# Kernel optimization log

Measured on AMD Instinct MI355X. Metric: run time of the kernel, lower is better.

Reference implementation:

```python
import jax, jax.numpy as jnp
import numpy as np

B, DIM, OC, H, W, HEADS = 4, 128, 128, 128, 128, 8
L = H * W
_BN_INV = 1.0 / (1.0 + 1e-5) ** 0.5  # eval-mode BN: running_mean=0, running_var=1


def conv2d(x, w, b=None, groups=1, pad=0):
    y = jax.lax.conv_general_dilated(
        x, w, (1, 1), [(pad, pad), (pad, pad)],
        dimension_numbers=('NCHW', 'OIHW', 'NCHW'),
        feature_group_count=groups)
    if b is not None:
        y = y + b[None, :, None, None]
    return y


def bn(x, g, b):
    return x * (g * _BN_INV)[None, :, None, None] + b[None, :, None, None]


def ln(x, g, b, eps=1e-5):
    m = jnp.mean(x, -1, keepdims=True)
    v = jnp.mean((x - m) ** 2, -1, keepdims=True)
    return (x - m) * jax.lax.rsqrt(v + eps) * g + b


def rope_tables(h, w, c, base=10000.0):
    k_max = c // 4
    theta = 1.0 / base ** (np.arange(k_max, dtype=np.float32) / k_max)
    gi, gj = np.meshgrid(np.arange(h, dtype=np.float32),
                         np.arange(w, dtype=np.float32), indexing='ij')
    ang = np.concatenate([gi[..., None] * theta, gj[..., None] * theta], -1)  # (h,w,c//2)
    return jnp.asarray(np.cos(ang)), jnp.asarray(np.sin(ang))


def apply_rope(x, cs, sn):  # x: (b,h,w,c); consecutive pairs = (re, im)
    xr, xi = x[..., 0::2], x[..., 1::2]
    return jnp.stack([cs * xr - sn * xi, sn * xr + cs * xi], -1).reshape(x.shape)


def linear_attn(x, qk_w, qk_b, lepe_w, lepe_b, h, w):
    b, n, c = x.shape
    hd = c // HEADS
    qk = x @ qk_w.T + qk_b
    q = jax.nn.elu(qk[..., :c]) + 1.0
    k = jax.nn.elu(qk[..., c:]) + 1.0
    cs, sn = rope_tables(h, w, c)

    def heads(t):  # (b,n,c) -> (b,HEADS,n,hd)
        return t.reshape(b, n, HEADS, hd).transpose(0, 2, 1, 3)

    q_r = heads(apply_rope(q.reshape(b, h, w, c), cs, sn).reshape(b, n, c))
    k_r = heads(apply_rope(k.reshape(b, h, w, c), cs, sn).reshape(b, n, c))
    qh, kh, vh = heads(q), heads(k), heads(x)
    k_mean = jnp.mean(kh, axis=2, keepdims=True)                      # (b,Hd,1,hd)
    z = 1.0 / (jnp.einsum('bhnd,bhmd->bhnm', qh, k_mean) + 1e-6)      # (b,Hd,n,1)
    s = n ** -0.5
    kv = jnp.einsum('bhnd,bhne->bhde', k_r * s, vh * s)               # (b,Hd,hd,hd)
    out = jnp.einsum('bhnd,bhde->bhne', q_r, kv) * z
    out = out.transpose(0, 2, 1, 3).reshape(b, n, c)
    v_img = x.reshape(b, h, w, c).transpose(0, 3, 1, 2)
    lepe = conv2d(v_img, lepe_w, lepe_b, groups=c, pad=1)
    return out + lepe.transpose(0, 2, 3, 1).reshape(b, n, c)


def fmt_block(xb, fw1, fb1, f_g, f_be, fw2, fb2, n_g, n_be):
    t = jnp.fft.fft2(xb)                                              # (B,C,H,W) complex
    wgt = jax.nn.relu(bn(conv2d(t.real, fw1, fb1), f_g, f_be))
    wgt = jax.nn.sigmoid(conv2d(wgt, fw2, fb2))
    f = jnp.abs(jnp.fft.ifft2(wgt * t))
    f = jax.nn.relu(bn(f, n_g, n_be))
    return f.reshape(f.shape[0], f.shape[1], -1).transpose(0, 2, 1)   # (B,L,C)


def _forward(x, c1_w, c1_b, c1_g, c1_be, cpe1_w, cpe1_b,
             fw1, fb1, f_g, f_be, fw2, fb2, nbn_g, nbn_be,
             ln1_g, ln1_b, d3w1, d3b1, d3w2, d5w1, d5b1, d5w2,
             ap_w, ap_b, ip2_w, ip2_b, dwc2_w, dwc2_b,
             qk_w, qk_b, lepe_w, lepe_b, op_w, op_b,
             cpe2_w, cpe2_b, ln2_g, ln2_b,
             ffn_w1, ffn_b1, ffn_w2, ffn_b2, po_w,
             red_w, red_b, red_g, red_be):
    Bb, C, Hh, Ww = x.shape
    Ll = Hh * Ww
    to_img = lambda t: t.reshape(Bb, Hh, Ww, C).transpose(0, 3, 1, 2)   # (B,L,C)->(B,C,H,W)
    to_seq = lambda t: t.transpose(0, 2, 3, 1).reshape(Bb, Ll, -1)       # (B,C,H,W)->(B,L,C)

    x_0 = jax.nn.relu(bn(conv2d(x, c1_w, c1_b), c1_g, c1_be))           # (B,OC,H,W)
    xt = to_seq(x + conv2d(x, cpe1_w, cpe1_b, groups=C, pad=1))
    shortcut = xt
    fmt1 = fmt_block(to_img(xt), fw1, fb1, f_g, f_be, fw2, fb2, nbn_g, nbn_be)

    x_s = ln(xt, ln1_g, ln1_b)
    xs_img = to_img(x_s)
    x_s3 = conv2d(conv2d(xs_img, d3w1, d3b1), d3w2, None, groups=C // 2, pad=1)
    x_s5 = conv2d(conv2d(xs_img, d5w1, d5b1), d5w2, None, groups=C // 2, pad=2)
    act_res = jax.nn.silu(to_seq(conv2d(xs_img, ap_w, ap_b)))

    def branch(t):  # (B,C/2,H,W) -> (B,L,C/2)
        t = conv2d(t, ip2_w, ip2_b)
        t = jax.nn.silu(conv2d(t, dwc2_w, dwc2_b, groups=C // 2, pad=1))
        return to_seq(t)

    a3 = linear_attn(branch(x_s3), qk_w, qk_b, lepe_w, lepe_b, Hh, Ww)
    a5 = linear_attn(branch(x_s5), qk_w, qk_b, lepe_w, lepe_b, Hh, Ww)
    xs = jnp.concatenate([a3, a5], -1)
    xs = to_seq(conv2d(to_img(xs * act_res), op_w, op_b))

    xt = shortcut + xs + fmt1
    xt = xt + to_seq(conv2d(to_img(xt), cpe2_w, cpe2_b, groups=C, pad=1))
    fmt2 = fmt_block(to_img(xt), fw1, fb1, f_g, f_be, fw2, fb2, nbn_g, nbn_be)
    h2 = ln(xt, ln2_g, ln2_b)
    ffn = jax.nn.gelu(h2 @ ffn_w1.T + ffn_b1, approximate=False) @ ffn_w2.T + ffn_b2
    xt = xt + ffn + fmt2

    xo = conv2d(to_img(xt), po_w)                                        # (B,OC,H,W)
    cat = jnp.concatenate([x_0, xo], 1)
    return jax.nn.relu(bn(conv2d(cat, red_w, red_b), red_g, red_be)) + x_0


def setup_inputs():
    key = jax.random.key(0)
    it = iter(jax.random.split(key, 64))

    def w(shape, s=0.05):
        return jax.random.normal(next(it), shape, jnp.float32) * s

    d, oc = DIM, OC
    ones = lambda n: jnp.ones((n,), jnp.float32)
    zeros = lambda n: jnp.zeros((n,), jnp.float32)
    return {
        'x': jax.random.normal(next(it), (B, d, H, W), jnp.float32),
        'c1_w': w((oc, d, 1, 1)), 'c1_b': w((oc,), 0.01), 'c1_g': ones(oc), 'c1_be': zeros(oc),
        'cpe1_w': w((d, 1, 3, 3)), 'cpe1_b': w((d,), 0.01),
        'fw1': w((d // 16, d, 1, 1)), 'fb1': w((d // 16,), 0.01),
        'f_g': ones(d // 16), 'f_be': zeros(d // 16),
        'fw2': w((d, d // 16, 1, 1)), 'fb2': w((d,), 0.01),
        'nbn_g': ones(d), 'nbn_be': zeros(d),
        'ln1_g': ones(d), 'ln1_b': zeros(d),
        'd3w1': w((d, d, 1, 1)), 'd3b1': w((d,), 0.01), 'd3w2': w((d // 2, 2, 3, 3)),
        'd5w1': w((d, d, 1, 1)), 'd5b1': w((d,), 0.01), 'd5w2': w((d // 2, 2, 5, 5)),
        'ap_w': w((d, d, 1, 1)), 'ap_b': w((d,), 0.01),
        'ip2_w': w((d // 2, d // 2, 1, 1)), 'ip2_b': w((d // 2,), 0.01),
        'dwc2_w': w((d // 2, 1, 3, 3)), 'dwc2_b': w((d // 2,), 0.01),
        'qk_w': w((d, d // 2)), 'qk_b': w((d,), 0.01),
        'lepe_w': w((d // 2, 1, 3, 3)), 'lepe_b': w((d // 2,), 0.01),
        'op_w': w((d, d, 1, 1)), 'op_b': w((d,), 0.01),
        'cpe2_w': w((d, 1, 3, 3)), 'cpe2_b': w((d,), 0.01),
        'ln2_g': ones(d), 'ln2_b': zeros(d),
        'ffn_w1': w((4, d)), 'ffn_b1': w((4,), 0.01),
        'ffn_w2': w((d, 4)), 'ffn_b2': w((d,), 0.01),
        'po_w': w((oc, d, 1, 1)),
        'red_w': w((oc, 2 * oc, 1, 1)), 'red_b': w((oc,), 0.01),
        'red_g': ones(oc), 'red_be': zeros(oc),
    }


def reference(x, c1_w, c1_b, c1_g, c1_be, cpe1_w, cpe1_b,
              fw1, fb1, f_g, f_be, fw2, fb2, nbn_g, nbn_be,
              ln1_g, ln1_b, d3w1, d3b1, d3w2, d5w1, d5b1, d5w2,
              ap_w, ap_b, ip2_w, ip2_b, dwc2_w, dwc2_b,
              qk_w, qk_b, lepe_w, lepe_b, op_w, op_b,
              cpe2_w, cpe2_b, ln2_g, ln2_b,
              ffn_w1, ffn_b1, ffn_w2, ffn_b2, po_w,
              red_w, red_b, red_g, red_be):
    return _forward(x, c1_w, c1_b, c1_g, c1_be, cpe1_w, cpe1_b,
                    fw1, fb1, f_g, f_be, fw2, fb2, nbn_g, nbn_be,
                    ln1_g, ln1_b, d3w1, d3b1, d3w2, d5w1, d5b1, d5w2,
                    ap_w, ap_b, ip2_w, ip2_b, dwc2_w, dwc2_b,
                    qk_w, qk_b, lepe_w, lepe_b, op_w, op_b,
                    cpe2_w, cpe2_b, ln2_g, ln2_b,
                    ffn_w1, ffn_b1, ffn_w2, ffn_b2, po_w,
                    red_w, red_b, red_g, red_be)
```

## Files before the change

kernel.cpp:

```cpp
#include <hip/hip_runtime.h>
#include <math.h>

typedef unsigned short bf16_t;
typedef __attribute__((ext_vector_type(8))) short short8;
typedef __attribute__((ext_vector_type(4))) float f32x4;

#define B_ 4
#define C_ 128
#define H_ 128
#define W_ 128
#define L_ (H_*W_)
#define NS  ((size_t)B_*L_*C_)
#define NH  ((size_t)B_*L_*64)
#define NSP ((size_t)L_*C_)
#define PI_F 3.14159265358979323846f
#define BN_INV 0.9999950000374997f
#define THETA_SC 0.8304820237218406f
#define TOTW 157148
#define W16SHIFT 107548

#define W2_ 66
#define L2_ (128*W2_)

__device__ __forceinline__ float ldf(bf16_t v){ return __uint_as_float(((unsigned)v)<<16); }
__device__ __forceinline__ bf16_t f2b(float f){
  unsigned u = __float_as_uint(f);
  u += 0x7fffu + ((u>>16)&1u);
  return (bf16_t)(u>>16);
}

#define WGSZ ((size_t)B_*8*L2_)
#define WGSLOT ((size_t)B_*8*L_)
#define ACCSZ 2304
#define CWSZ 157184
#define CW16SZF 78592
#define WSF (6*NS + 3*NH + WGSLOT + ACCSZ + CWSZ + CW16SZF + 16)
__device__ float g_ws[WSF];

__global__ void k_probe(const bf16_t* __restrict__ xb, int* __restrict__ flag){
  __shared__ int vote;
  if (threadIdx.x == 0) vote = 0;
  __syncthreads();
  int bad = 0;
  for (int i = threadIdx.x; i < 2048; i += 256) {
    float v = ldf(xb[2*i]);
    if (!(fabsf(v) < 1e6f)) bad = 1;
  }
  if (bad) atomicOr(&vote, 1);
  __syncthreads();
  if (threadIdx.x == 0) *flag = vote;
}

struct P47 { const void* p[47]; };
__device__ __constant__ int c_wsz[47] = {
  16384,128,128,128,1152,128,1024,8,8,8,1024,128,128,128,128,128,
  16384,128,1152,16384,128,3200,16384,128,4096,64,576,64,8192,128,
  576,64,16384,128,1152,128,128,128,512,4,512,128,16384,32768,128,128,128};

__global__ __launch_bounds__(256) void k_cvt(P47 ps, const int* __restrict__ flagp,
                                             float* __restrict__ dst){
  int g = blockIdx.x*256 + threadIdx.x;
  if (g >= TOTW) return;
  int fl = *flagp;
  int idx = 0, off = g;
  while (off >= c_wsz[idx]) { off -= c_wsz[idx]; idx++; }
  const void* s = ps.p[idx];
  dst[g] = fl ? ((const float*)s)[off] : ldf(((const bf16_t*)s)[off]);
}

__global__ __launch_bounds__(256) void k_cvt16(const float* __restrict__ src, bf16_t* __restrict__ dst){
  int g = blockIdx.x*256 + threadIdx.x;
  if (g >= TOTW) return;
  dst[g + (g >= W16SHIFT ? 4 : 0)] = f2b(src[g]);
}

__global__ void k_zero(float* p, int n){
  int i = blockIdx.x*256 + threadIdx.x;
  if (i < n) p[i] = 0.f;
}

__device__ __forceinline__ void tw_fwd(int lane, float* tc, float* ts) {
  sincosf(-PI_F * (float)lane * (1.f/64.f), &ts[0], &tc[0]);
  int i = 1;
  #pragma unroll
  for (int m = 32; m >= 1; m >>= 1, i++) {
    int k = lane & (m-1);
    sincosf(-PI_F * (float)k / (float)m, &ts[i], &tc[i]);
  }
}
__device__ __forceinline__ void tw_inv(int lane, float* tc, float* ts) {
  int i = 0;
  #pragma unroll
  for (int m = 1; m <= 32; m <<= 1, i++) {
    int k = lane & (m-1);
    sincosf(PI_F * (float)k / (float)m, &ts[i], &tc[i]);
  }
  sincosf(PI_F * (float)lane * (1.f/64.f), &ts[6], &tc[6]);
}

__device__ __forceinline__ void fft128_fwd(float& lor, float& loi, float& hir, float& hii,
                                           int lane, const float* tc, const float* ts) {
  {
    float s = ts[0], c = tc[0];
    float ar = lor, ai = loi;
    float dr = ar - hir, di = ai - hii;
    lor = ar + hir; loi = ai + hii;
    hir = dr*c - di*s; hii = dr*s + di*c;
  }
  int i = 1;
  #pragma unroll
  for (int m = 32; m >= 1; m >>= 1, i++) {
    float s = ts[i], c = tc[i];
    bool up = (lane & m) != 0;
    {
      float orr = __shfl_xor(lor, m), oii = __shfl_xor(loi, m);
      float sr = lor + orr, si = loi + oii;
      float dr = orr - lor, di = oii - loi;
      float tr = dr*c - di*s, ti = dr*s + di*c;
      lor = up ? tr : sr; loi = up ? ti : si;
    }
    {
      float orr = __shfl_xor(hir, m), oii = __shfl_xor(hii, m);
      float sr = hir + orr, si = hii + oii;
      float dr = orr - hir, di = oii - hii;
      float tr = dr*c - di*s, ti = dr*s + di*c;
      hir = up ? tr : sr; hii = up ? ti : si;
    }
  }
}

__device__ __forceinline__ void fft128_inv(float& lor, float& loi, float& hir, float& hii,
                                           int lane, const float* tc, const float* ts) {
  int i = 0;
  #pragma unroll
  for (int m = 1; m <= 32; m <<= 1, i++) {
    float s = ts[i], c = tc[i];
    bool up = (lane & m) != 0;
    {
      float orr = __shfl_xor(lor, m), oii = __shfl_xor(loi, m);
      float qr = orr*c - oii*s, qi = orr*s + oii*c;
      float lo_r = lor + qr, lo_i = loi + qi;
      float mr = lor*c - loi*s, mi = lor*s + loi*c;
      float up_r = orr - mr, up_i = oii - mi;
      lor = up ? up_r : lo_r; loi = up ? up_i : lo_i;
    }
    {
      float orr = __shfl_xor(hir, m), oii = __shfl_xor(hii, m);
      float qr = orr*c - oii*s, qi = orr*s + oii*c;
      float lo_r = hir + qr, lo_i = hii + qi;
      float mr = hir*c - hii*s, mi = hir*s + hii*c;
      float up_r = orr - mr, up_i = oii - mi;
      hir = up ? up_r : lo_r; hii = up ? up_i : lo_i;
    }
  }
  {
    float s = ts[6], c = tc[6];
    float qr = hir*c - hii*s, qi = hir*s + hii*c;
    float pr = lor, pi = loi;
    lor = pr + qr; loi = pi + qi;
    hir = pr - qr; hii = pi - qi;
  }
}

__global__ __launch_bounds__(256) void k_fft_row_fwd_half(
    const float* __restrict__ in, float* __restrict__ re, float* __restrict__ im) {
  __shared__ float T[64*130];
  int tid = threadIdx.x;
  int bid = blockIdx.x;
  int ch = (bid & 1) * 64;
  int h  = (bid >> 1) & 127;
  int b  = bid >> 8;
  const float* ip = in + ((size_t)b*L_ + (size_t)h*128)*128 + ch;
  #pragma unroll
  for (int it = 0; it < 8; it++) {
    int idx = it*256 + tid;
    int c4 = (idx & 15)*4, w = idx >> 4;
    float4 v = *(const float4*)(ip + (size_t)w*128 + c4);
    T[(c4+0)*130 + w] = v.x;
    T[(c4+1)*130 + w] = v.y;
    T[(c4+2)*130 + w] = v.z;
    T[(c4+3)*130 + w] = v.w;
  }
  __syncthreads();
  int lane = tid & 63, wv = tid >> 6;
  int rb = (int)(__brev((unsigned)lane) >> 26);
  int pe = (64 - lane) & 63;
  int po = 63 - lane;
  float tc[7], ts[7];
  tw_fwd(lane, tc, ts);
  #pragma unroll
  for (int t = 0; t < 8; t++) {
    int ca = wv*16 + 2*t, cb = ca + 1;
    float lor = T[ca*130 + lane],      loi = T[cb*130 + lane];
    float hir = T[ca*130 + 64 + lane], hii = T[cb*130 + 64 + lane];
    fft128_fwd(lor, loi, hir, hii, lane, tc, ts);
    float er  = __shfl(lor, rb), ei  = __shfl(loi, rb);
    float our = __shfl(hir, rb), oui = __shfl(hii, rb);
    float per = __shfl(er, pe),  pei = __shfl(ei, pe);
    float por = __shfl(our, po), poi = __shfl(oui, po);
    float ae_r = 0.5f*(er + per),  ae_i = 0.5f*(ei - pei);
    float be_r = 0.5f*(ei + pei),  be_i = 0.5f*(per - er);
    float ao_r = 0.5f*(our + por), ao_i = 0.5f*(oui - poi);
    float bo_r = 0.5f*(oui + poi), bo_i = 0.5f*(por - our);
    if (lane == 32) { ao_r = 0.f; ao_i = 0.f; bo_r = 0.f; bo_i = 0.f; }
    if (lane <= 32) {
      size_t ba = (size_t)(b*128 + ch + ca)*L2_ + (size_t)h*W2_ + 2*lane;
      size_t bb = (size_t)(b*128 + ch + cb)*L2_ + (size_t)h*W2_ + 2*lane;
      *(float2*)(re + ba) = make_float2(ae_r, ao_r);
      *(float2*)(im + ba) = make_float2(ae_i, ao_i);
      *(float2*)(re + bb) = make_float2(be_r, bo_r);
      *(float2*)(im + bb) = make_float2(be_i, bo_i);
    }
  }
}

__global__ __launch_bounds__(256) void k_fft_col_fwd_h(float* __restrict__ re, float* __restrict__ im) {
  __shared__ float Lre[128][34];
  __shared__ float Lim[128][34];
  int tid = threadIdx.x;
  size_t img = blockIdx.x >> 1;
  int w0 = (blockIdx.x & 1) * 33;
  float* rp = re + img * (size_t)L2_ + w0;
  float* ip = im + img * (size_t)L2_ + w0;
  for (int i = tid; i < 4224; i += 256) {
    int h = i / 33, wl = i - h*33;
    Lre[h][wl] = rp[(size_t)h*W2_ + wl];
    Lim[h][wl] = ip[(size_t)h*W2_ + wl];
  }
  __syncthreads();
  int lane = tid & 63, wv = tid >> 6;
  float tc[7], ts[7];
  tw_fwd(lane, tc, ts);
  for (int col = wv; col < 33; col += 4) {
    float lor = Lre[lane][col], loi = Lim[lane][col];
    float hir = Lre[lane+64][col], hii = Lim[lane+64][col];
    fft128_fwd(lor, loi, hir, hii, lane, tc, ts);
    Lre[lane][col]=lor; Lim[lane][col]=loi;
    Lre[lane+64][col]=hir; Lim[lane+64][col]=hii;
  }
  __syncthreads();
  for (int i = tid; i < 4224; i += 256) {
    int h = i / 33, wl = i - h*33;
    rp[(size_t)h*W2_ + wl] = Lre[h][wl];
    ip[(size_t)h*W2_ + wl] = Lim[h][wl];
  }
}

__global__ __launch_bounds__(256) void k_fft_col_inv_scaled_h(
    float* __restrict__ re, float* __restrict__ im,
    const float* __restrict__ wg1, const float* __restrict__ fw2,
    const float* __restrict__ fb2) {
  __shared__ float Lre[128][34];
  __shared__ float Lim[128][34];
  __shared__ float w2r[8];
  int tid = threadIdx.x;
  size_t img = blockIdx.x >> 1;
  int c = (int)(img & 127);
  int b = (int)(img >> 7);
  int w0 = (blockIdx.x & 1) * 33;
  if (tid < 8) w2r[tid] = fw2[c*8 + tid];
  float b2 = fb2[c];
  float* rp = re + img * (size_t)L2_ + w0;
  float* ip = im + img * (size_t)L2_ + w0;
  const float* wgp = wg1 + (size_t)b*8*L2_ + w0;
  __syncthreads();
  for (int i = tid; i < 4224; i += 256) {
    int h = i / 33, wl = i - h*33;
    size_t p = (size_t)h*W2_ + wl;
    float a = b2;
    #pragma unroll
    for (int o = 0; o < 8; o++) a += w2r[o] * wgp[(size_t)o*L2_ + p];
    float wgt = 1.f/(1.f+expf(-a));
    Lre[h][wl] = rp[p] * wgt;
    Lim[h][wl] = ip[p] * wgt;
  }
  __syncthreads();
  int lane = tid & 63, wv = tid >> 6;
  float tc[7], ts[7];
  tw_inv(lane, tc, ts);
  for (int col = wv; col < 33; col += 4) {
    float lor = Lre[lane][col], loi = Lim[lane][col];
    float hir = Lre[lane+64][col], hii = Lim[lane+64][col];
    fft128_inv(lor, loi, hir, hii, lane, tc, ts);
    Lre[lane][col]=lor*(1.f/128.f); Lim[lane][col]=loi*(1.f/128.f);
    Lre[lane+64][col]=hir*(1.f/128.f); Lim[lane+64][col]=hii*(1.f/128.f);
  }
  __syncthreads();
  for (int i = tid; i < 4224; i += 256) {
    int h = i / 33, wl = i - h*33;
    rp[(size_t)h*W2_ + wl] = Lre[h][wl];
    ip[(size_t)h*W2_ + wl] = Lim[h][wl];
  }
}

__global__ __launch_bounds__(256) void k_fft_row_inv_abs_seq_h(
    const float* __restrict__ re, const float* __restrict__ im,
    const float* __restrict__ ng, const float* __restrict__ nbe,
    const float* __restrict__ add1, const float* __restrict__ add2,
    float* __restrict__ out) {
  __shared__ float S[64*132];
  int tid = threadIdx.x;
  int bid = blockIdx.x;
  int ch = (bid & 1) * 64;
  int h  = (bid >> 1) & 127;
  int b  = bid >> 8;
  {
    const float* rbase = re + (size_t)(b*128 + ch)*L2_ + (size_t)h*W2_;
    const float* ibase = im + (size_t)(b*128 + ch)*L2_ + (size_t)h*W2_;
    for (int i = tid; i < 64*66; i += 256) {
      int c = i / 66, v = i - c*66;
      S[c*132 + v]      = rbase[(size_t)c*L2_ + v];
      S[c*132 + 66 + v] = ibase[(size_t)c*L2_ + v];
    }
  }
  __syncthreads();
  int lane = tid & 63, wv = tid >> 6;
  int rb = (int)(__brev((unsigned)lane) >> 26);
  int vlo = 2*rb, vhi = vlo + 1;
  float tc[7], ts[7];
  tw_inv(lane, tc, ts);
  float rr[8][4];
  #pragma unroll
  for (int t = 0; t < 8; t++) {
    int ca = wv*16 + 2*t, cb = ca + 1;
    const float* Sa = S + ca*132;
    const float* Sb = S + cb*132;
    float lor, loi, hir, hii;
    if (vlo <= 64) {
      float ar = Sa[vlo], ai = Sa[66+vlo], br = Sb[vlo], bi = Sb[66+vlo];
      lor = ar - bi; loi = ai + br;
    } else {
      int u = 128 - vlo;
      float ar = Sa[u], ai = Sa[66+u], br = Sb[u], bi = Sb[66+u];
      lor = ar + bi; loi = br - ai;
    }
    if (vhi <= 64) {
      float ar = Sa[vhi], ai = Sa[66+vhi], br = Sb[vhi], bi = Sb[66+vhi];
      hir = ar - bi; hii = ai + br;
    } else {
      int u = 128 - vhi;
      float ar = Sa[u], ai = Sa[66+u], br = Sb[u], bi = Sb[66+u];
      hir = ar + bi; hii = br - ai;
    }
    fft128_inv(lor, loi, hir, hii, lane, tc, ts);
    rr[t][0] = fabsf(lor);
    rr[t][1] = fabsf(loi);
    rr[t][2] = fabsf(hir);
    rr[t][3] = fabsf(hii);
  }
  __syncthreads();
  float* T = S;
  #pragma unroll
  for (int t = 0; t < 8; t++) {
    int ca = wv*16 + 2*t, cb = ca + 1;
    float sga = ng[ch+ca]*BN_INV, sba = nbe[ch+ca];
    float sgb = ng[ch+cb]*BN_INV, sbb = nbe[ch+cb];
    T[ca*130 + lane]      = fmaxf(rr[t][0]*(1.f/128.f)*sga + sba, 0.f);
    T[cb*130 + lane]      = fmaxf(rr[t][1]*(1.f/128.f)*sgb + sbb, 0.f);
    T[ca*130 + 64 + lane] = fmaxf(rr[t][2]*(1.f/128.f)*sga + sba, 0.f);
    T[cb*130 + 64 + lane] = fmaxf(rr[t][3]*(1.f/128.f)*sgb + sbb, 0.f);
  }
  __syncthreads();
  size_t sb0 = ((size_t)b*L_ + (size_t)h*128)*128 + ch;
  #pragma unroll
  for (int it = 0; it < 8; it++) {
    int idx = it*256 + tid;
    int c4 = (idx & 15)*4, w = idx >> 4;
    size_t off = sb0 + (size_t)w*128 + c4;
    float4 v;
    v.x = T[(c4+0)*130 + w];
    v.y = T[(c4+1)*130 + w];
    v.z = T[(c4+2)*130 + w];
    v.w = T[(c4+3)*130 + w];
    float4 x1 = *(const float4*)(add1 + off);
    float4 x2 = *(const float4*)(add2 + off);
    v.x += x1.x + x2.x; v.y += x1.y + x2.y;
    v.z += x1.z + x2.z; v.w += x1.w + x2.w;
    *(float4*)(out + off) = v;
  }
}

__global__ __launch_bounds__(256) void k_freq1_h(const float* __restrict__ tre,
    const float* __restrict__ fw1, const float* __restrict__ fb1,
    const float* __restrict__ fg, const float* __restrict__ fbe,
    float* __restrict__ wg1) {
  __shared__ float w1s[1024];
  int tid = threadIdx.x;
  for (int i = tid; i < 1024; i += 256) w1s[i] = fw1[i];
  __syncthreads();
  size_t g = (size_t)blockIdx.x*256 + tid;
  int p = (int)(g % L2_);
  int b = (int)(g / L2_);
  const float* tp = tre + (size_t)b*128*L2_ + p;
  float acc[8];
  #pragma unroll
  for (int o = 0; o < 8; o++) acc[o] = 0.f;
  for (int c = 0; c < 128; c++) {
    float v = tp[(size_t)c*L2_];
    #pragma unroll
    for (int o = 0; o < 8; o++) acc[o] += w1s[o*128+c]*v;
  }
  size_t ob = (size_t)b*8*L2_ + p;
  #pragma unroll
  for (int o = 0; o < 8; o++) {
    float v = (acc[o] + fb1[o]) * (fg[o]*BN_INV) + fbe[o];
    wg1[ob + (size_t)o*L2_] = fmaxf(v, 0.f);
  }
}

template<bool DUAL>
__global__ void k_p2s(const void* __restrict__ src, float* __restrict__ dst,
                      const float* __restrict__ add1, const float* __restrict__ add2,
                      const int* __restrict__ flagp) {
  __shared__ float tile[32][33];
  int fl = DUAL ? *flagp : 1;
  int b = blockIdx.z;
  int p0 = blockIdx.x*32, c0 = blockIdx.y*32;
  int tx = threadIdx.x, ty = threadIdx.y;
  size_t base_in = (size_t)b*NSP;
  #pragma unroll
  for (int k = 0; k < 4; k++) {
    size_t off = base_in + (size_t)(c0+ty+8*k)*L_ + p0 + tx;
    float v;
    if (DUAL && !fl) v = ldf(((const bf16_t*)src)[off]);
    else             v = ((const float*)src)[off];
    tile[ty+8*k][tx] = v;
  }
  __syncthreads();
  size_t base = (size_t)b*NSP;
  #pragma unroll
  for (int k = 0; k < 4; k++) {
    size_t idx = base + (size_t)(p0+ty+8*k)*C_ + c0 + tx;
    float v = tile[tx][ty+8*k];
    if (add1) v += add1[idx];
    if (add2) v += add2[idx];
    dst[idx] = v;
  }
}

template<int CC, int MODE>
__global__ __launch_bounds__(256) void k_dw3(const float* __restrict__ in,
    const float* __restrict__ w, const float* __restrict__ bias,
    float* __restrict__ out) {
  __shared__ float wl[9*CC];
  int tid = threadIdx.x;
  for (int i = tid; i < 9*CC; i += 256) {
    int tap = i / CC, ch = i % CC;
    wl[i] = w[ch*9 + tap];
  }
  __syncthreads();
  size_t g = (size_t)blockIdx.x*256 + tid;
  int c = (int)(g & (CC-1));
  float wr[9];
  #pragma unroll
  for (int t = 0; t < 9; t++) wr[t] = wl[t*CC + c];
  size_t s = g / CC;
  int w0 = (int)(s & 31) * 4;
  int hp = (int)((s >> 5) & 127);
  int b  = (int)(s >> 12);
  const float* ip = in + (size_t)b*L_*CC + c;
  float bi = bias[c];
  float a0 = bi, a1 = bi, a2 = bi, a3 = bi;
  #pragma unroll
  for (int dh = -1; dh <= 1; dh++) {
    int h2 = hp + dh;
    if ((unsigned)h2 >= 128u) continue;
    const float* rp = ip + (size_t)h2*W_*CC;
    float px[6];
    #pragma unroll
    for (int x = 0; x < 6; x++) {
      int w2 = w0 - 1 + x;
      px[x] = ((unsigned)w2 < 128u) ? rp[(size_t)w2*CC] : 0.f;
    }
    #pragma unroll
    for (int dw = 0; dw < 3; dw++) {
      float f = wr[(dh+1)*3 + dw];
      a0 += f*px[dw];   a1 += f*px[dw+1];
      a2 += f*px[dw+2]; a3 += f*px[dw+3];
    }
  }
  size_t tb = (size_t)b*L_ + (size_t)hp*W_ + w0;
  if (MODE == 0) {
    out[(tb+0)*CC + c] = in[(tb+0)*CC + c] + a0;
    out[(tb+1)*CC + c] = in[(tb+1)*CC + c] + a1;
    out[(tb+2)*CC + c] = in[(tb+2)*CC + c] + a2;
    out[(tb+3)*CC + c] = in[(tb+3)*CC + c] + a3;
  } else {
    out[(tb+0)*CC + c] = a0 / (1.f + expf(-a0));
    out[(tb+1)*CC + c] = a1 / (1.f + expf(-a1));
    out[(tb+2)*CC + c] = a2 / (1.f + expf(-a2));
    out[(tb+3)*CC + c] = a3 / (1.f + expf(-a3));
  }
}

template<int K>
__global__ __launch_bounds__(256) void k_gconv(const float* __restrict__ in,
    const float* __restrict__ w, float* __restrict__ out) {
  __shared__ float wl[K*K*128];
  int tid = threadIdx.x;
  for (int i = tid; i < 128*K*K; i += 256) {
    int tap = i >> 7, ch = i & 127;
    wl[i] = w[ch*(K*K) + tap];
  }
  __syncthreads();
  size_t g = (size_t)blockIdx.x*256 + tid;
  int oc = (int)(g & 63);
  float wx[K*K], wy[K*K];
  #pragma unroll
  for (int t = 0; t < K*K; t++) {
    wx[t] = wl[t*128 + 2*oc];
    wy[t] = wl[t*128 + 2*oc + 1];
  }
  size_t s = g >> 6;
  int w0 = (int)(s & 31) * 4;
  int hp = (int)((s >> 5) & 127);
  int b  = (int)(s >> 12);
  const float* ip = in + (size_t)b*L_*128 + 2*oc;
  constexpr int P = K/2;
  float a0 = 0.f, a1 = 0.f, a2 = 0.f, a3 = 0.f;
  #pragma unroll
  for (int kh = 0; kh < K; kh++) {
    int h2 = hp + kh - P;
    if ((unsigned)h2 >= 128u) continue;
    const float* rp = ip + (size_t)h2*W_*128;
    float2 px[K+3];
    #pragma unroll
    for (int x = 0; x < K+3; x++) {
      int w2 = w0 - P + x;
      px[x] = ((unsigned)w2 < 128u) ? *(const float2*)(rp + (size_t)w2*128)
                                    : make_float2(0.f, 0.f);
    }
    #pragma unroll
    for (int kw = 0; kw < K; kw++) {
      float fx = wx[kh*K + kw], fy = wy[kh*K + kw];
      a0 += fx*px[kw+0].x + fy*px[kw+0].y;
      a1 += fx*px[kw+1].x + fy*px[kw+1].y;
      a2 += fx*px[kw+2].x + fy*px[kw+2].y;
      a3 += fx*px[kw+3].x + fy*px[kw+3].y;
    }
  }
  size_t tb = (size_t)b*L_ + (size_t)hp*W_ + w0;
  out[(tb+0)*64 + oc] = a0;
  out[(tb+1)*64 + oc] = a1;
  out[(tb+2)*64 + oc] = a2;
  out[(tb+3)*64 + oc] = a3;
}

template<int CIN, int COUT, int EPI, bool MUL>
__global__ __launch_bounds__(256) void k_mfma_tok(
    const float* __restrict__ in, const float* __restrict__ mulp,
    const bf16_t* __restrict__ W16, const float* __restrict__ bias,
    float* __restrict__ out) {
  constexpr int NO = COUT/16;
  int tid = threadIdx.x;
  int lane = tid & 63, wv = tid >> 6;
  int m = lane & 15, q = lane >> 4;
  size_t t0 = (size_t)blockIdx.x*64 + (size_t)wv*16;
  f32x4 acc[NO];
  #pragma unroll
  for (int i = 0; i < NO; i++) acc[i] = (f32x4){0.f,0.f,0.f,0.f};
  for (int k0 = 0; k0 < CIN; k0 += 32) {
    const float* ap = in + (t0 + m)*CIN + k0 + q*8;
    float4 a0 = *(const float4*)ap;
    float4 a1 = *(const float4*)(ap + 4);
    if (MUL) {
      const float* mp = mulp + (t0 + m)*CIN + k0 + q*8;
      float4 m0 = *(const float4*)mp;
      float4 m1 = *(const float4*)(mp + 4);
      a0.x*=m0.x; a0.y*=m0.y; a0.z*=m0.z; a0.w*=m0.w;
      a1.x*=m1.x; a1.y*=m1.y; a1.z*=m1.z; a1.w*=m1.w;
    }
    union { short s[8]; short8 v; } af;
    af.s[0]=(short)f2b(a0.x); af.s[1]=(short)f2b(a0.y);
    af.s[2]=(short)f2b(a0.z); af.s[3]=(short)f2b(a0.w);
    af.s[4]=(short)f2b(a1.x); af.s[5]=(short)f2b(a1.y);
    af.s[6]=(short)f2b(a1.z); af.s[7]=(short)f2b(a1.w);
    #pragma unroll
    for (int o = 0; o < NO; o++) {
      short8 bf = *(const short8*)(W16 + (size_t)(o*16 + m)*CIN + k0 + q*8);
      acc[o] = __builtin_amdgcn_mfma_f32_16x16x32_bf16(af.v, bf, acc[o], 0, 0, 0);
    }
  }
  #pragma unroll
  for (int o = 0; o < NO; o++) {
    float bv = (EPI >= 1) ? bias[o*16 + m] : 0.f;
    #pragma unroll
    for (int r = 0; r < 4; r++) {
      int row = q*4 + r;
      float v = acc[o][r] + bv;
      if (EPI == 2) v = v / (1.f + expf(-v));
      if (EPI == 3) v = v > 0.f ? v + 1.f : expf(v);
      out[(t0 + row)*COUT + o*16 + m] = v;
    }
  }
}

__global__ __launch_bounds__(256) void k_mfma_c1(
    const float* __restrict__ in, const bf16_t* __restrict__ W16,
    const float* __restrict__ bias, const float* __restrict__ gam,
    const float* __restrict__ bet, float* __restrict__ out) {
  constexpr int NO = 8;
  int tid = threadIdx.x;
  int lane = tid & 63, wv = tid >> 6;
  int m = lane & 15, q = lane >> 4;
  size_t t0 = (size_t)blockIdx.x*64 + (size_t)wv*16;
  f32x4 acc[NO];
  #pragma unroll
  for (int i = 0; i < NO; i++) acc[i] = (f32x4){0.f,0.f,0.f,0.f};
  for (int k0 = 0; k0 < 128; k0 += 32) {
    const float* ap = in + (t0 + m)*128 + k0 + q*8;
    float4 a0 = *(const float4*)ap;
    float4 a1 = *(const float4*)(ap + 4);
    union { short s[8]; short8 v; } af;
    af.s[0]=(short)f2b(a0.x); af.s[1]=(short)f2b(a0.y);
    af.s[2]=(short)f2b(a0.z); af.s[3]=(short)f2b(a0.w);
    af.s[4]=(short)f2b(a1.x); af.s[5]=(short)f2b(a1.y);
    af.s[6]=(short)f2b(a1.z); af.s[7]=(short)f2b(a1.w);
    #pragma unroll
    for (int o = 0; o < NO; o++) {
      short8 bf = *(const short8*)(W16 + (size_t)(o*16 + m)*128 + k0 + q*8);
      acc[o] = __builtin_amdgcn_mfma_f32_16x16x32_bf16(af.v, bf, acc[o], 0, 0, 0);
    }
  }
  #pragma unroll
  for (int o = 0; o < NO; o++) {
    int oc = o*16 + m;
    float bi = bias[oc], gm = gam[oc]*BN_INV, be = bet[oc];
    #pragma unroll
    for (int r = 0; r < 4; r++) {
      int row = q*4 + r;
      float v = acc[o][r] + bi;
      out[(t0 + row)*128 + oc] = fmaxf(v*gm + be, 0.f);
    }
  }
}

__global__ __launch_bounds__(256) void k_mfma_red(
    const float* __restrict__ x0s, const float* __restrict__ xo,
    const bf16_t* __restrict__ W16, const float* __restrict__ bias,
    const float* __restrict__ gam, const float* __restrict__ bet,
    void* __restrict__ out, const int* __restrict__ flagp) {
  __shared__ float T[128*65];
  constexpr int NO = 8;
  int fl = *flagp;
  int tid = threadIdx.x;
  int lane = tid & 63, wv = tid >> 6;
  int m = lane & 15, q = lane >> 4;
  size_t t0 = (size_t)blockIdx.x*64;
  size_t tw = t0 + (size_t)wv*16;
  f32x4 acc[NO];
  #pragma unroll
  for (int i = 0; i < NO; i++) acc[i] = (f32x4){0.f,0.f,0.f,0.f};
  for (int k0 = 0; k0 < 256; k0 += 32) {
    const float* src = (k0 < 128) ? (x0s + (tw + m)*128 + k0)
                                  : (xo  + (tw + m)*128 + (k0 - 128));
    float4 a0 = *(const float4*)(src + q*8);
    float4 a1 = *(const float4*)(src + q*8 + 4);
    union { short s[8]; short8 v; } af;
    af.s[0]=(short)f2b(a0.x); af.s[1]=(short)f2b(a0.y);
    af.s[2]=(short)f2b(a0.z); af.s[3]=(short)f2b(a0.w);
    af.s[4]=(short)f2b(a1.x); af.s[5]=(short)f2b(a1.y);
    af.s[6]=(short)f2b(a1.z); af.s[7]=(short)f2b(a1.w);
    #pragma unroll
    for (int o = 0; o < NO; o++) {
      short8 bf = *(const short8*)(W16 + (size_t)(o*16 + m)*256 + k0 + q*8);
      acc[o] = __builtin_amdgcn_mfma_f32_16x16x32_bf16(af.v, bf, acc[o], 0, 0, 0);
    }
  }
  #pragma unroll
  for (int ot = 0; ot < NO; ot++) {
    int o = ot*16 + m;
    float bi = bias[o], gm = gam[o]*BN_INV, be = bet[o];
    #pragma unroll
    for (int r = 0; r < 4; r++) {
      int row = q*4 + r;
      float v = acc[ot][r] + bi;
      v = fmaxf(v*gm + be, 0.f);
      v += x0s[(tw + row)*128 + o];
      T[o*65 + wv*16 + row] = v;
    }
  }
  __syncthreads();
  int b = (int)(t0 >> 14);
  int p0 = (int)(t0 & (L_-1));
  if (!fl) {
    bf16_t* op = (bf16_t*)out;
    for (int i = tid; i < 8192; i += 256) {
      int o = i >> 6, tk = i & 63;
      op[((size_t)b*128 + o)*L_ + p0 + tk] = f2b(T[o*65 + tk]);
    }
  } else {
    float* op = (float*)out;
    for (int i = tid; i < 8192; i += 256) {
      int o = i >> 6, tk = i & 63;
      op[((size_t)b*128 + o)*L_ + p0 + tk] = T[o*65 + tk];
    }
  }
}

__global__ __launch_bounds__(256) void k_ln(const float* __restrict__ in,
    const float* __restrict__ g, const float* __restrict__ be, float* __restrict__ out) {
  int tid = threadIdx.x, lane = tid & 63;
  size_t t = (size_t)blockIdx.x*4 + (tid >> 6);
  const float* row = in + t*128;
  float2 v = *(const float2*)(row + lane*2);
  float s = v.x + v.y, ss = v.x*v.x + v.y*v.y;
  #pragma unroll
  for (int m = 1; m < 64; m <<= 1) { s += __shfl_xor(s, m); ss += __shfl_xor(ss, m); }
  float mean = s*(1.f/128.f);
  float inv = rsqrtf(ss*(1.f/128.f) - mean*mean + 1e-5f);
  float2 o;
  o.x = (v.x-mean)*inv*g[lane*2]   + be[lane*2];
  o.y = (v.y-mean)*inv*g[lane*2+1] + be[lane*2+1];
  *(float2*)(out + t*128 + lane*2) = o;
}

__global__ __launch_bounds__(256) void k_ln_ffn(const float* __restrict__ in,
    const float* __restrict__ g, const float* __restrict__ be,
    const float* __restrict__ w1, const float* __restrict__ b1,
    const float* __restrict__ w2, const float* __restrict__ b2,
    float* __restrict__ out) {
  int tid = threadIdx.x, lane = tid & 63;
  size_t t = (size_t)blockIdx.x*4 + (tid >> 6);
  const float* row = in + t*128;
  float2 v = *(const float2*)(row + lane*2);
  float s = v.x + v.y, ss = v.x*v.x + v.y*v.y;
  #pragma unroll
  for (int m = 1; m < 64; m <<= 1) { s += __shfl_xor(s, m); ss += __shfl_xor(ss, m); }
  float mean = s*(1.f/128.f);
  float inv = rsqrtf(ss*(1.f/128.f) - mean*mean + 1e-5f);
  float hx = (v.x-mean)*inv*g[lane*2]   + be[lane*2];
  float hy = (v.y-mean)*inv*g[lane*2+1] + be[lane*2+1];
  float hp0 = hx*w1[0*128+lane*2] + hy*w1[0*128+lane*2+1];
  float hp1 = hx*w1[1*128+lane*2] + hy*w1[1*128+lane*2+1];
  float hp2 = hx*w1[2*128+lane*2] + hy*w1[2*128+lane*2+1];
  float hp3 = hx*w1[3*128+lane*2] + hy*w1[3*128+lane*2+1];
  #pragma unroll
  for (int m = 1; m < 64; m <<= 1) {
    hp0 += __shfl_xor(hp0, m); hp1 += __shfl_xor(hp1, m);
    hp2 += __shfl_xor(hp2, m); hp3 += __shfl_xor(hp3, m);
  }
  float hv0, hv1, hv2, hv3;
  { float a = hp0 + b1[0]; hv0 = 0.5f*a*(1.f+erff(a*0.7071067811865476f)); }
  { float a = hp1 + b1[1]; hv1 = 0.5f*a*(1.f+erff(a*0.7071067811865476f)); }
  { float a = hp2 + b1[2]; hv2 = 0.5f*a*(1.f+erff(a*0.7071067811865476f)); }
  { float a = hp3 + b1[3]; hv3 = 0.5f*a*(1.f+erff(a*0.7071067811865476f)); }
  int cx = lane*2, cy = lane*2+1;
  float2 o;
  o.x = hv0*w2[cx*4+0] + hv1*w2[cx*4+1] + hv2*w2[cx*4+2] + hv3*w2[cx*4+3] + b2[cx];
  o.y = hv0*w2[cy*4+0] + hv1*w2[cy*4+1] + hv2*w2[cy*4+2] + hv3*w2[cy*4+3] + b2[cy];
  *(float2*)(out + t*128 + lane*2) = o;
}

__global__ __launch_bounds__(256) void k_kv(
    const float* __restrict__ qk, const float* __restrict__ v,
    float* __restrict__ akv_g, float* __restrict__ aks_g) {
  __shared__ float kvred[512];
  __shared__ float ksred[64];
  int tid = threadIdx.x;
  for (int i = tid; i < 512; i += 256) kvred[i] = 0.f;
  if (tid < 64) ksred[tid] = 0.f;
  __syncthreads();
  int lane = tid & 63, wv = tid >> 6;
  size_t t0 = (size_t)blockIdx.x * 64;
  int b = (int)(t0 >> 14);
  int pr = lane >> 1;
  float theta = exp2f(-(float)(pr & 15) * THETA_SC);
  bool use_i = pr < 16;
  int hbase = lane & 56;
  float akv[8];
  #pragma unroll
  for (int d = 0; d < 8; d++) akv[d] = 0.f;
  float aks = 0.f;
  for (int it = 0; it < 16; it++) {
    size_t t = t0 + (size_t)wv*16 + it;
    float k = qk[t*128 + 64 + lane];
    float xv = v[t*64 + lane];
    int l = (int)(t & (L_-1));
    float pos = use_i ? (float)(l >> 7) : (float)(l & 127);
    float sn, cs; sincosf(pos*theta, &sn, &cs);
    float kp = __shfl_xor(k, 1);
    float kr = (lane & 1) ? (sn*kp + cs*k) : (cs*k - sn*kp);
    #pragma unroll
    for (int d = 0; d < 8; d++) {
      float krd = __shfl(kr, hbase + d);
      akv[d] += krd * xv;
    }
    aks += k;
  }
  int h8 = lane >> 3, e = lane & 7;
  #pragma unroll
  for (int d = 0; d < 8; d++)
    atomicAdd(&kvred[h8*64 + d*8 + e], akv[d]);
  atomicAdd(&ksred[lane], aks);
  __syncthreads();
  for (int i = tid; i < 512; i += 256) atomicAdd(&akv_g[b*512 + i], kvred[i]);
  if (tid < 64) atomicAdd(&aks_g[b*64 + tid], ksred[tid]);
}

__global__ __launch_bounds__(256) void k_attn2(
    const float* __restrict__ qk, const float* __restrict__ x,
    const float* __restrict__ akv_g, const float* __restrict__ aks_g,
    const float* __restrict__ lw, const float* __restrict__ lb,
    float* __restrict__ out, int coff) {
  __shared__ float kv[512];
  __shared__ float km[64];
  __shared__ float lwl[576];
  int tid = threadIdx.x;
  size_t t0 = (size_t)blockIdx.x * 32;
  int b = (int)(t0 >> 14);
  const float invn = 1.f/16384.f;
  for (int i = tid; i < 512; i += 256) kv[i] = akv_g[b*512 + i]*invn;
  if (tid < 64) km[tid] = aks_g[b*64 + tid]*invn;
  for (int i = tid; i < 576; i += 256) lwl[i] = lw[i];
  __syncthreads();
  int lane = tid & 63, wv = tid >> 6;
  int pr = lane >> 1;
  float theta = exp2f(-(float)(pr & 15) * THETA_SC);
  bool use_i = pr < 16;
  int hbase = lane & 56, e = lane & 7;
  float lbv = lb[lane];
  const float* xb = x + ((size_t)b << 14) * 64;
  for (int it = 0; it < 8; it++) {
    size_t t = t0 + (size_t)wv*8 + it;
    int l = (int)(t & (L_-1));
    int ipos = l >> 7, jpos = l & 127;
    float q = qk[t*128 + lane];
    float p = q * km[lane];
    p += __shfl_xor(p, 1); p += __shfl_xor(p, 2); p += __shfl_xor(p, 4);
    float z = 1.f/(p + 1e-6f);
    float pos = use_i ? (float)ipos : (float)jpos;
    float sn, cs; sincosf(pos*theta, &sn, &cs);
    float qp = __shfl_xor(q, 1);
    float qr = (lane & 1) ? (sn*qp + cs*q) : (cs*q - sn*qp);
    float acc = 0.f;
    #pragma unroll
    for (int d = 0; d < 8; d++) {
      float qrd = __shfl(qr, hbase + d);
      acc += qrd * kv[hbase*8 + d*8 + e];
    }
    acc *= z;
    float lp = lbv;
    #pragma unroll
    for (int dh = -1; dh <= 1; dh++) {
      int h2 = ipos + dh; if ((unsigned)h2 >= 128u) continue;
      #pragma unroll
      for (int dw = -1; dw <= 1; dw++) {
        int w2 = jpos + dw; if ((unsigned)w2 >= 128u) continue;
        lp += lwl[lane*9 + (dh+1)*3 + (dw+1)] * xb[((size_t)(h2 << 7) + w2)*64 + lane];
      }
    }
    out[t*128 + coff + lane] = acc + lp;
  }
}

extern "C" void kernel_launch(void* const* d_in, const int* in_sizes, int n_in,
                              void* d_out, int out_size, void* d_ws, size_t ws_size,
                              hipStream_t stream) {
  (void)in_sizes; (void)n_in; (void)out_size;

  float* base;
  if (ws_size >= WSF * sizeof(float)) {
    base = (float*)d_ws;
  } else {
    void* p = nullptr;
    hipGetSymbolAddress(&p, HIP_SYMBOL(g_ws));
    base = (float*)p;
  }
  float* P0 = base;
  float* PA = base + 1*NS;
  float* PB = base + 2*NS;
  float* PC = base + 3*NS;
  float* PD = base + 4*NS;
  float* PF = base + 5*NS;
  float* H0 = base + 6*NS;
  float* H1 = H0 + NH;
  float* H2 = H1 + NH;
  float* WG = H2 + NH;
  float* ACC = WG + WGSLOT;
  float* CW  = ACC + ACCSZ;
  bf16_t* CW16 = (bf16_t*)(CW + CWSZ);
  int*   FLG = (int*)(CW + CWSZ + CW16SZF);

  static const int wsz[47] = {
    16384,128,128,128,1152,128,1024,8,8,8,1024,128,128,128,128,128,
    16384,128,1152,16384,128,3200,16384,128,4096,64,576,64,8192,128,
    576,64,16384,128,1152,128,128,128,512,4,512,128,16384,32768,128,128,128};
  int woff[47]; { int a = 0; for (int i = 0; i < 47; i++){ woff[i] = a; a += wsz[i]; } }
  const float* Wf[47]; for (int i = 0; i < 47; i++) Wf[i] = CW + woff[i];
  auto W16 = [&](int i){ return (const bf16_t*)(CW16 + woff[i] + (woff[i] >= W16SHIFT ? 4 : 0)); };
  const float *c1_b=Wf[1], *c1_g=Wf[2], *c1_be=Wf[3], *cpe1_w=Wf[4],
    *cpe1_b=Wf[5], *fw1=Wf[6], *fb1=Wf[7], *f_g=Wf[8], *f_be=Wf[9], *fw2=Wf[10],
    *fb2=Wf[11], *nbn_g=Wf[12], *nbn_be=Wf[13], *ln1_g=Wf[14], *ln1_b=Wf[15],
    *d3b1=Wf[17], *d3w2=Wf[18], *d5b1=Wf[20],
    *d5w2=Wf[21], *ap_b=Wf[23], *ip2_b=Wf[25],
    *dwc2_w=Wf[26], *dwc2_b=Wf[27], *qk_b=Wf[29], *lepe_w=Wf[30],
    *lepe_b=Wf[31], *op_b=Wf[33], *cpe2_w=Wf[34], *cpe2_b=Wf[35],
    *ln2_g=Wf[36], *ln2_b=Wf[37], *ffn_w1=Wf[38], *ffn_b1=Wf[39], *ffn_w2=Wf[40],
    *ffn_b2=Wf[41], *red_b=Wf[44], *red_g=Wf[45], *red_be=Wf[46];
  const bf16_t *c1_w16=W16(0), *d3w1_16=W16(16), *d5w1_16=W16(19), *ap_w16=W16(22),
    *ip2_w16=W16(24), *qk_w16=W16(28), *op_w16=W16(32), *po_w16=W16(42), *red_w16=W16(43);

  const void* x = d_in[0];

  k_probe<<<1, 256, 0, stream>>>((const bf16_t*)x, FLG);
  P47 ps; for (int i = 0; i < 47; i++) ps.p[i] = d_in[i+1];
  k_cvt<<<(TOTW+255)/256, 256, 0, stream>>>(ps, FLG, CW);
  k_cvt16<<<(TOTW+255)/256, 256, 0, stream>>>(CW, CW16);

  dim3 tgrid(512, 4, 4), tblk(32, 8);

  auto fmt_fused = [&](const float* seq_in, float* re, float* im,
                       const float* add1, const float* add2, float* outp) {
    k_fft_row_fwd_half<<<1024, 256, 0, stream>>>(seq_in, re, im);
    k_fft_col_fwd_h<<<1024, 256, 0, stream>>>(re, im);
    k_freq1_h<<<132, 256, 0, stream>>>(re, fw1, fb1, f_g, f_be, WG);
    k_fft_col_inv_scaled_h<<<1024, 256, 0, stream>>>(re, im, WG, fw2, fb2);
    k_fft_row_inv_abs_seq_h<<<1024, 256, 0, stream>>>(re, im, nbn_g, nbn_be, add1, add2, outp);
  };

  auto attn = [&](const float* brin, float* qkbuf, int coff) {
    k_zero<<<9, 256, 0, stream>>>(ACC, 2304);
    k_mfma_tok<64,128,3,false><<<1024, 256, 0, stream>>>(brin, nullptr, qk_w16, qk_b, qkbuf);
    k_kv<<<1024, 256, 0, stream>>>(qkbuf, brin, ACC, ACC + B_*512);
    k_attn2<<<2048, 256, 0, stream>>>(qkbuf, brin, ACC, ACC + B_*512, lepe_w, lepe_b, PF, coff);
  };

  k_p2s<true><<<tgrid, tblk, 0, stream>>>(x, PA, nullptr, nullptr, FLG);
  k_mfma_c1<<<1024, 256, 0, stream>>>(PA, c1_w16, c1_b, c1_g, c1_be, P0);
  k_dw3<128,0><<<8192, 256, 0, stream>>>(PA, cpe1_w, cpe1_b, PB);
  k_ln<<<16384, 256, 0, stream>>>(PB, ln1_g, ln1_b, PA);
  k_mfma_tok<128,128,1,false><<<1024, 256, 0, stream>>>(PA, nullptr, d3w1_16, d3b1, PD);
  k_gconv<3><<<4096, 256, 0, stream>>>(PD, d3w2, H0);
  k_mfma_tok<128,128,1,false><<<1024, 256, 0, stream>>>(PA, nullptr, d5w1_16, d5b1, PD);
  k_gconv<5><<<4096, 256, 0, stream>>>(PD, d5w2, H1);
  k_mfma_tok<128,128,2,false><<<1024, 256, 0, stream>>>(PA, nullptr, ap_w16, ap_b, PA);
  k_mfma_tok<64,64,1,false><<<1024, 256, 0, stream>>>(H0, nullptr, ip2_w16, ip2_b, H2);
  k_dw3<64,1><<<4096, 256, 0, stream>>>(H2, dwc2_w, dwc2_b, H0);
  attn(H0, PD, 0);
  k_mfma_tok<64,64,1,false><<<1024, 256, 0, stream>>>(H1, nullptr, ip2_w16, ip2_b, H2);
  k_dw3<64,1><<<4096, 256, 0, stream>>>(H2, dwc2_w, dwc2_b, H1);
  attn(H1, PD, 64);
  k_mfma_tok<128,128,1,true><<<1024, 256, 0, stream>>>(PF, PA, op_w16, op_b, PF);
  fmt_fused(PB, PC, PD, PB, PF, PB);
  k_dw3<128,0><<<8192, 256, 0, stream>>>(PB, cpe2_w, cpe2_b, PC);
  k_ln_ffn<<<16384, 256, 0, stream>>>(PC, ln2_g, ln2_b, ffn_w1, ffn_b1, ffn_w2, ffn_b2, PF);
  fmt_fused(PC, PB, PD, PC, PF, PC);
  k_mfma_tok<128,128,0,false><<<1024, 256, 0, stream>>>(PC, nullptr, po_w16, nullptr, PD);
  k_mfma_red<<<1024, 256, 0, stream>>>(P0, PD, red_w16, red_b, red_g, red_be, d_out, FLG);
}
```

Before: 975.4 us.

## Fold po projection into reduction weights and batch activation loads in MFMA kernels

Precomputes the product of the second half of the reduction 1x1 conv weights with the po projection weights, so the final reduction consumes the FMT output directly. This drops one full token GEMM launch and its intermediate buffer write and read. Separately, the MFMA token kernels now issue all K-chunk activation loads up front before converting and multiplying, which raises memory-level parallelism at some register cost. The composed weight is rounded to bf16 once, which slightly changes numerics compared with two sequential bf16 GEMMs.

```diff
diff --git a/kernel.cpp b/kernel.cpp
--- a/kernel.cpp
+++ b/kernel.cpp
@@ -18,6 +18,8 @@
 #define THETA_SC 0.8304820237218406f
 #define TOTW 157148
 #define W16SHIFT 107548
+#define WOFF_PO 107612
+#define WOFF_RED 123996
 
 #define W2_ 66
 #define L2_ (128*W2_)
@@ -29,7 +31,6 @@
   return (bf16_t)(u>>16);
 }
 
-#define WGSZ ((size_t)B_*8*L2_)
 #define WGSLOT ((size_t)B_*8*L_)
 #define ACCSZ 2304
 #define CWSZ 157184
@@ -72,6 +73,15 @@
   int g = blockIdx.x*256 + threadIdx.x;
   if (g >= TOTW) return;
   dst[g + (g >= W16SHIFT ? 4 : 0)] = f2b(src[g]);
+}
+
+__global__ __launch_bounds__(256) void k_fuse_red(const float* __restrict__ po,
+    const float* __restrict__ rw, bf16_t* __restrict__ dst16){
+  int g = blockIdx.x*256 + threadIdx.x;
+  int o = g >> 7, in = g & 127;
+  float acc = 0.f;
+  for (int j = 0; j < 128; j++) acc += rw[o*256 + 128 + j] * po[j*128 + in];
+  dst16[o*256 + 128 + in] = f2b(acc);
 }
 
 __global__ void k_zero(float* p, int n){
@@ -552,6 +562,7 @@
     const bf16_t* __restrict__ W16, const float* __restrict__ bias,
     float* __restrict__ out) {
   constexpr int NO = COUT/16;
+  constexpr int KS = (CIN >= 128) ? 4 : (CIN/32);
   int tid = threadIdx.x;
   int lane = tid & 63, wv = tid >> 6;
   int m = lane & 15, q = lane >> 4;
@@ -559,26 +570,36 @@
   f32x4 acc[NO];
   #pragma unroll
   for (int i = 0; i < NO; i++) acc[i] = (f32x4){0.f,0.f,0.f,0.f};
-  for (int k0 = 0; k0 < CIN; k0 += 32) {
-    const float* ap = in + (t0 + m)*CIN + k0 + q*8;
-    float4 a0 = *(const float4*)ap;
-    float4 a1 = *(const float4*)(ap + 4);
+  for (int kc = 0; kc < CIN; kc += KS*32) {
+    float4 A[KS][2];
+    #pragma unroll
+    for (int kk = 0; kk < KS; kk++) {
+      const float* ap = in + (t0 + m)*CIN + kc + kk*32 + q*8;
+      A[kk][0] = *(const float4*)ap;
+      A[kk][1] = *(const float4*)(ap + 4);
+    }
     if (MUL) {
-      const float* mp = mulp + (t0 + m)*CIN + k0 + q*8;
-      float4 m0 = *(const float4*)mp;
-      float4 m1 = *(const float4*)(mp + 4);
-      a0.x*=m0.x; a0.y*=m0.y; a0.z*=m0.z; a0.w*=m0.w;
-      a1.x*=m1.x; a1.y*=m1.y; a1.z*=m1.z; a1.w*=m1.w;
-    }
-    union { short s[8]; short8 v; } af;
-    af.s[0]=(short)f2b(a0.x); af.s[1]=(short)f2b(a0.y);
-    af.s[2]=(short)f2b(a0.z); af.s[3]=(short)f2b(a0.w);
-    af.s[4]=(short)f2b(a1.x); af.s[5]=(short)f2b(a1.y);
-    af.s[6]=(short)f2b(a1.z); af.s[7]=(short)f2b(a1.w);
-    #pragma unroll
-    for (int o = 0; o < NO; o++) {
-      short8 bf = *(const short8*)(W16 + (size_t)(o*16 + m)*CIN + k0 + q*8);
-      acc[o] = __builtin_amdgcn_mfma_f32_16x16x32_bf16(af.v, bf, acc[o], 0, 0, 0);
+      #pragma unroll
+      for (int kk = 0; kk < KS; kk++) {
+        const float* mp = mulp + (t0 + m)*CIN + kc + kk*32 + q*8;
+        float4 m0 = *(const float4*)mp;
+        float4 m1 = *(const float4*)(mp + 4);
+        A[kk][0].x*=m0.x; A[kk][0].y*=m0.y; A[kk][0].z*=m0.z; A[kk][0].w*=m0.w;
+        A[kk][1].x*=m1.x; A[kk][1].y*=m1.y; A[kk][1].z*=m1.z; A[kk][1].w*=m1.w;
+      }
+    }
+    #pragma unroll
+    for (int kk = 0; kk < KS; kk++) {
+      union { short s[8]; short8 v; } af;
+      af.s[0]=(short)f2b(A[kk][0].x); af.s[1]=(short)f2b(A[kk][0].y);
+      af.s[2]=(short)f2b(A[kk][0].z); af.s[3]=(short)f2b(A[kk][0].w);
+      af.s[4]=(short)f2b(A[kk][1].x); af.s[5]=(short)f2b(A[kk][1].y);
+      af.s[6]=(short)f2b(A[kk][1].z); af.s[7]=(short)f2b(A[kk][1].w);
+      #pragma unroll
+      for (int o = 0; o < NO; o++) {
+        short8 bf = *(const short8*)(W16 + (size_t)(o*16 + m)*CIN + kc + kk*32 + q*8);
+        acc[o] = __builtin_amdgcn_mfma_f32_16x16x32_bf16(af.v, bf, acc[o], 0, 0, 0);
+      }
     }
   }
   #pragma unroll
@@ -607,19 +628,26 @@
   f32x4 acc[NO];
   #pragma unroll
   for (int i = 0; i < NO; i++) acc[i] = (f32x4){0.f,0.f,0.f,0.f};
-  for (int k0 = 0; k0 < 128; k0 += 32) {
-    const float* ap = in + (t0 + m)*128 + k0 + q*8;
-    float4 a0 = *(const float4*)ap;
-    float4 a1 = *(const float4*)(ap + 4);
-    union { short s[8]; short8 v; } af;
-    af.s[0]=(short)f2b(a0.x); af.s[1]=(short)f2b(a0.y);
-    af.s[2]=(short)f2b(a0.z); af.s[3]=(short)f2b(a0.w);
-    af.s[4]=(short)f2b(a1.x); af.s[5]=(short)f2b(a1.y);
-    af.s[6]=(short)f2b(a1.z); af.s[7]=(short)f2b(a1.w);
-    #pragma unroll
-    for (int o = 0; o < NO; o++) {
-      short8 bf = *(const short8*)(W16 + (size_t)(o*16 + m)*128 + k0 + q*8);
-      acc[o] = __builtin_amdgcn_mfma_f32_16x16x32_bf16(af.v, bf, acc[o], 0, 0, 0);
+  {
+    float4 A[4][2];
+    #pragma unroll
+    for (int kk = 0; kk < 4; kk++) {
+      const float* ap = in + (t0 + m)*128 + kk*32 + q*8;
+      A[kk][0] = *(const float4*)ap;
+      A[kk][1] = *(const float4*)(ap + 4);
+    }
+    #pragma unroll
+    for (int kk = 0; kk < 4; kk++) {
+      union { short s[8]; short8 v; } af;
+      af.s[0]=(short)f2b(A[kk][0].x); af.s[1]=(short)f2b(A[kk][0].y);
+      af.s[2]=(short)f2b(A[kk][0].z); af.s[3]=(short)f2b(A[kk][0].w);
+      af.s[4]=(short)f2b(A[kk][1].x); af.s[5]=(short)f2b(A[kk][1].y);
+      af.s[6]=(short)f2b(A[kk][1].z); af.s[7]=(short)f2b(A[kk][1].w);
+      #pragma unroll
+      for (int o = 0; o < NO; o++) {
+        short8 bf = *(const short8*)(W16 + (size_t)(o*16 + m)*128 + kk*32 + q*8);
+        acc[o] = __builtin_amdgcn_mfma_f32_16x16x32_bf16(af.v, bf, acc[o], 0, 0, 0);
+      }
     }
   }
   #pragma unroll
@@ -636,7 +664,7 @@
 }
 
 __global__ __launch_bounds__(256) void k_mfma_red(
-    const float* __restrict__ x0s, const float* __restrict__ xo,
+    const float* __restrict__ x0s, const float* __restrict__ xt4,
     const bf16_t* __restrict__ W16, const float* __restrict__ bias,
     const float* __restrict__ gam, const float* __restrict__ bet,
     void* __restrict__ out, const int* __restrict__ flagp) {
@@ -651,20 +679,28 @@
   f32x4 acc[NO];
   #pragma unroll
   for (int i = 0; i < NO; i++) acc[i] = (f32x4){0.f,0.f,0.f,0.f};
-  for (int k0 = 0; k0 < 256; k0 += 32) {
-    const float* src = (k0 < 128) ? (x0s + (tw + m)*128 + k0)
-                                  : (xo  + (tw + m)*128 + (k0 - 128));
-    float4 a0 = *(const float4*)(src + q*8);
-    float4 a1 = *(const float4*)(src + q*8 + 4);
-    union { short s[8]; short8 v; } af;
-    af.s[0]=(short)f2b(a0.x); af.s[1]=(short)f2b(a0.y);
-    af.s[2]=(short)f2b(a0.z); af.s[3]=(short)f2b(a0.w);
-    af.s[4]=(short)f2b(a1.x); af.s[5]=(short)f2b(a1.y);
-    af.s[6]=(short)f2b(a1.z); af.s[7]=(short)f2b(a1.w);
-    #pragma unroll
-    for (int o = 0; o < NO; o++) {
-      short8 bf = *(const short8*)(W16 + (size_t)(o*16 + m)*256 + k0 + q*8);
-      acc[o] = __builtin_amdgcn_mfma_f32_16x16x32_bf16(af.v, bf, acc[o], 0, 0, 0);
+  #pragma unroll
+  for (int half = 0; half < 2; half++) {
+    const float* src = half ? xt4 : x0s;
+    float4 A[4][2];
+    #pragma unroll
+    for (int kk = 0; kk < 4; kk++) {
+      const float* ap = src + (tw + m)*128 + kk*32 + q*8;
+      A[kk][0] = *(const float4*)ap;
+      A[kk][1] = *(const float4*)(ap + 4);
+    }
+    #pragma unroll
+    for (int kk = 0; kk < 4; kk++) {
+      union { short s[8]; short8 v; } af;
+      af.s[0]=(short)f2b(A[kk][0].x); af.s[1]=(short)f2b(A[kk][0].y);
+      af.s[2]=(short)f2b(A[kk][0].z); af.s[3]=(short)f2b(A[kk][0].w);
+      af.s[4]=(short)f2b(A[kk][1].x); af.s[5]=(short)f2b(A[kk][1].y);
+      af.s[6]=(short)f2b(A[kk][1].z); af.s[7]=(short)f2b(A[kk][1].w);
+      #pragma unroll
+      for (int o = 0; o < NO; o++) {
+        short8 bf = *(const short8*)(W16 + (size_t)(o*16 + m)*256 + half*128 + kk*32 + q*8);
+        acc[o] = __builtin_amdgcn_mfma_f32_16x16x32_bf16(af.v, bf, acc[o], 0, 0, 0);
+      }
     }
   }
   #pragma unroll
@@ -899,7 +935,7 @@
     *ln2_g=Wf[36], *ln2_b=Wf[37], *ffn_w1=Wf[38], *ffn_b1=Wf[39], *ffn_w2=Wf[40],
     *ffn_b2=Wf[41], *red_b=Wf[44], *red_g=Wf[45], *red_be=Wf[46];
   const bf16_t *c1_w16=W16(0), *d3w1_16=W16(16), *d5w1_16=W16(19), *ap_w16=W16(22),
-    *ip2_w16=W16(24), *qk_w16=W16(28), *op_w16=W16(32), *po_w16=W16(42), *red_w16=W16(43);
+    *ip2_w16=W16(24), *qk_w16=W16(28), *op_w16=W16(32), *red_w16=W16(43);
 
   const void* x = d_in[0];
 
@@ -907,6 +943,8 @@
   P47 ps; for (int i = 0; i < 47; i++) ps.p[i] = d_in[i+1];
   k_cvt<<<(TOTW+255)/256, 256, 0, stream>>>(ps, FLG, CW);
   k_cvt16<<<(TOTW+255)/256, 256, 0, stream>>>(CW, CW16);
+  k_fuse_red<<<64, 256, 0, stream>>>(CW + WOFF_PO, CW + WOFF_RED,
+                                     (bf16_t*)(CW16 + WOFF_RED + 4));
 
   dim3 tgrid(512, 4, 4), tblk(32, 8);
 
@@ -946,6 +984,5 @@
   k_dw3<128,0><<<8192, 256, 0, stream>>>(PB, cpe2_w, cpe2_b, PC);
   k_ln_ffn<<<16384, 256, 0, stream>>>(PC, ln2_g, ln2_b, ffn_w1, ffn_b1, ffn_w2, ffn_b2, PF);
   fmt_fused(PC, PB, PD, PC, PF, PC);
-  k_mfma_tok<128,128,0,false><<<1024, 256, 0, stream>>>(PC, nullptr, po_w16, nullptr, PD);
-  k_mfma_red<<<1024, 256, 0, stream>>>(P0, PD, red_w16, red_b, red_g, red_be, d_out, FLG);
-}
+  k_mfma_red<<<1024, 256, 0, stream>>>(P0, PC, red_w16, red_b, red_g, red_be, d_out, FLG);
+}
```

Result: no change. 965.6 us (-1.0%).
